# Kernel optimization log

Measured on AMD Instinct MI355X. Metric: run time of the kernel, lower is better.

The kernel has to match this reference:

```python
import jax, jax.numpy as jnp
import numpy as np

INPUT, HIDDEN, OUT = 30, 128, 11

def setup_inputs() -> dict:
    key = jax.random.key(0)
    ks = jax.random.split(key, 9)
    s_ih = 1.0 / np.sqrt(HIDDEN)
    def u(k, shape):
        return jax.random.uniform(k, shape, jnp.float32, -s_ih, s_ih)
    return {
        "x": jax.random.normal(ks[0], (4096, 256, INPUT), jnp.float32),
        "W_ih": u(ks[1], (4 * HIDDEN, INPUT)),
        "W_hh": u(ks[2], (4 * HIDDEN, HIDDEN)),
        "b_ih": u(ks[3], (4 * HIDDEN,)),
        "b_hh": u(ks[4], (4 * HIDDEN,)),
        "W0": u(ks[5], (HIDDEN, HIDDEN)),
        "b0": u(ks[6], (HIDDEN,)),
        "W1": u(ks[7], (OUT, HIDDEN)),
        "b1": u(ks[8], (OUT,)),
    }

def lstm_last_h(x, W_ih, W_hh, b_ih, b_hh):
    # x: [B, T, I]; precompute input projections for all timesteps
    B = x.shape[0]
    xg = jnp.einsum('bti,gi->btg', x, W_ih) + b_ih + b_hh  # [B, T, 4H]
    def step(carry, g_x):
        h, c = carry
        g = g_x + h @ W_hh.T  # [B, 4H]
        i, f, gg, o = jnp.split(g, 4, axis=-1)  # PyTorch gate order i,f,g,o
        i = jax.nn.sigmoid(i); f = jax.nn.sigmoid(f)
        gg = jnp.tanh(gg); o = jax.nn.sigmoid(o)
        c = f * c + i * gg
        h = o * jnp.tanh(c)
        return (h, c), None
    h0 = jnp.zeros((B, HIDDEN), x.dtype)
    c0 = jnp.zeros((B, HIDDEN), x.dtype)
    (h, c), _ = jax.lax.scan(step, (h0, c0), jnp.swapaxes(xg, 0, 1))
    return h

def reference(x, W_ih, W_hh, b_ih, b_hh, W0, b0, W1, b1):
    h = lstm_last_h(x, W_ih, W_hh, b_ih, b_hh)  # [B, H]
    y0 = jax.nn.relu(h @ W0.T + b0)
    return y0 @ W1.T + b1  # [B, 11]
```

## Files before the change

kernel.cpp:

```cpp
#include <hip/hip_runtime.h>

#define TT 256
#define II 30
#define HH 128
#define TB 16
#define HROWF 136
#define XROWF 40
#define XTT 16
#define XPANEL (XTT * TB * XROWF)

typedef _Float16 half8 __attribute__((ext_vector_type(8)));
typedef _Float16 half2v __attribute__((ext_vector_type(2)));
typedef float f32x4 __attribute__((ext_vector_type(4)));

#if __has_builtin(__builtin_amdgcn_exp2f)
#define EXP2(x) __builtin_amdgcn_exp2f(x)
#else
#define EXP2(x) exp2f(x)
#endif
#define RCP(x) __builtin_amdgcn_rcpf(x)

#define L2E 1.44269504089f
#define TWO_L2E 2.88539008177f

__device__ __forceinline__ float sig2(float a) {
  return RCP(1.0f + EXP2(-a));
}
__device__ __forceinline__ float tanh2(float a) {
  return fmaf(-2.0f, RCP(1.0f + EXP2(a)), 1.0f);
}
__device__ __forceinline__ float tanh2s(float c) {
  return tanh2(c * TWO_L2E);
}

__global__ __launch_bounds__(512, 2)
void lstm_mfma(const float* __restrict__ x,
               const float* __restrict__ W_ih,
               const float* __restrict__ W_hh,
               const float* __restrict__ b_ih,
               const float* __restrict__ b_hh,
               const float* __restrict__ W0,
               const float* __restrict__ b0v,
               const float* __restrict__ W1,
               const float* __restrict__ b1v,
               float* __restrict__ out)
{
  __shared__ __align__(16) _Float16 Hb[2][TB * HROWF];
  __shared__ __align__(16) _Float16 Xp[2][XPANEL];
  __shared__ float y0ls[TB * 132];

  const int tid = threadIdx.x;
  const int bbase = blockIdx.x * TB;
  const int wv = tid >> 6;
  const int lane = tid & 63;
  const int col = lane & 15;
  const int grp = lane >> 4;

  half8 bf[4][5];
  float bias[4];
  #pragma unroll
  for (int g = 0; g < 4; ++g) {
    const float sc = (g == 2) ? TWO_L2E : L2E;
    const int n = g * 128 + wv * 16 + col;
    #pragma unroll
    for (int ks = 0; ks < 4; ++ks) {
      const float4 p = *reinterpret_cast<const float4*>(W_hh + n * HH + ks * 32 + grp * 8);
      const float4 q = *reinterpret_cast<const float4*>(W_hh + n * HH + ks * 32 + grp * 8 + 4);
      bf[g][ks] = (half8){(_Float16)(p.x * sc), (_Float16)(p.y * sc),
                          (_Float16)(p.z * sc), (_Float16)(p.w * sc),
                          (_Float16)(q.x * sc), (_Float16)(q.y * sc),
                          (_Float16)(q.z * sc), (_Float16)(q.w * sc)};
    }
    {
      float v[8];
      #pragma unroll
      for (int j = 0; j < 8; ++j) {
        const int cc = grp * 8 + j;
        v[j] = (cc < II) ? W_ih[n * II + cc] * sc : 0.0f;
      }
      bf[g][4] = (half8){(_Float16)v[0], (_Float16)v[1], (_Float16)v[2], (_Float16)v[3],
                         (_Float16)v[4], (_Float16)v[5], (_Float16)v[6], (_Float16)v[7]};
    }
    bias[g] = (b_ih[n] + b_hh[n]) * sc;
  }

  const bool stg = (tid < 480);
  const int sS = stg ? (tid / 30) : 15;
  const int qS = tid % 30;
  const int g0 = qS * 16;
  const int tt0 = g0 / 30;
  const int i00 = g0 % 30;
  const float* wbase = x + (size_t)(bbase + sS) * (TT * II);

  float4 xr0, xr1, xr2, xr3;
  auto xload = [&](int win) {
    if (!stg) return;
    const float* p = wbase + win * (XTT * II) + g0;
    xr0 = *reinterpret_cast<const float4*>(p);
    xr1 = *reinterpret_cast<const float4*>(p + 4);
    xr2 = *reinterpret_cast<const float4*>(p + 8);
    xr3 = *reinterpret_cast<const float4*>(p + 12);
  };
  auto xwrite = [&](int dstb) {
    if (!stg) return;
    _Float16* d = &Xp[dstb][0];
    const float vv[16] = {xr0.x, xr0.y, xr0.z, xr0.w, xr1.x, xr1.y, xr1.z, xr1.w,
                          xr2.x, xr2.y, xr2.z, xr2.w, xr3.x, xr3.y, xr3.z, xr3.w};
    int tt = tt0, i = i00;
    #pragma unroll
    for (int j = 0; j < 16; ++j) {
      d[tt * (TB * XROWF) + sS * XROWF + i] = (_Float16)vv[j];
      ++i;
      if (i == II) { i = 0; ++tt; }
    }
  };

  if (tid < 256) {
    const int s = tid >> 4, u8 = (tid & 15) * 8;
    *reinterpret_cast<half8*>(&Hb[0][s * HROWF + u8]) = (half8){0,0,0,0,0,0,0,0};
  }
  {
    const int pb = tid >> 8, rr = tid & 255;
    const int tt = rr >> 4, s = rr & 15;
    *reinterpret_cast<half2v*>(&Xp[pb][tt * (TB * XROWF) + s * XROWF + II]) = (half2v){0, 0};
  }

  float c[4] = {0.0f, 0.0f, 0.0f, 0.0f};

  xload(0);
  xwrite(0);
  __syncthreads();

  auto step = [&](int tt_idx, const _Float16* Ar, _Float16* Aw, const _Float16* Xr) {
    half8 af[5];
    #pragma unroll
    for (int ks = 0; ks < 4; ++ks)
      af[ks] = *reinterpret_cast<const half8*>(&Ar[col * HROWF + ks * 32 + grp * 8]);
    af[4] = *reinterpret_cast<const half8*>(&Xr[tt_idx * (TB * XROWF) + col * XROWF + grp * 8]);

    f32x4 a0 = {bias[0], bias[0], bias[0], bias[0]};
    f32x4 a1 = {bias[1], bias[1], bias[1], bias[1]};
    #pragma unroll
    for (int ks = 0; ks < 5; ++ks)
      a0 = __builtin_amdgcn_mfma_f32_16x16x32_f16(af[ks], bf[0][ks], a0, 0, 0, 0);
    #pragma unroll
    for (int ks = 0; ks < 5; ++ks)
      a1 = __builtin_amdgcn_mfma_f32_16x16x32_f16(af[ks], bf[1][ks], a1, 0, 0, 0);

    float ig[4], fg[4];
    #pragma unroll
    for (int r = 0; r < 4; ++r) { ig[r] = sig2(a0[r]); fg[r] = sig2(a1[r]); }

    f32x4 a2 = {bias[2], bias[2], bias[2], bias[2]};
    f32x4 a3 = {bias[3], bias[3], bias[3], bias[3]};
    #pragma unroll
    for (int ks = 0; ks < 5; ++ks)
      a2 = __builtin_amdgcn_mfma_f32_16x16x32_f16(af[ks], bf[2][ks], a2, 0, 0, 0);
    #pragma unroll
    for (int ks = 0; ks < 5; ++ks)
      a3 = __builtin_amdgcn_mfma_f32_16x16x32_f16(af[ks], bf[3][ks], a3, 0, 0, 0);

    #pragma unroll
    for (int r = 0; r < 4; ++r) {
      const float tg = tanh2(a2[r]);
      const float og = sig2(a3[r]);
      const float cn = fmaf(fg[r], c[r], ig[r] * tg);
      c[r] = cn;
      Aw[(grp * 4 + r) * HROWF + wv * 16 + col] = (_Float16)(og * tanh2s(cn));
    }
    __syncthreads();
  };

  for (int win = 0; win < 16; ++win) {
    const _Float16* Xr = Xp[win & 1];
    if (win + 1 < 16) xload(win + 1);
    for (int k = 0; k < 8; k += 2) {
      step(k,     Hb[0], Hb[1], Xr);
      step(k + 1, Hb[1], Hb[0], Xr);
    }
    if (win + 1 < 16) xwrite((win + 1) & 1);
    for (int k = 8; k < 16; k += 2) {
      step(k,     Hb[0], Hb[1], Xr);
      step(k + 1, Hb[1], Hb[0], Xr);
    }
  }

  if (tid < 256) {
    const int s = tid >> 4;
    const int n0 = (tid & 15) * 8;
    float acch[8];
    #pragma unroll
    for (int nj = 0; nj < 8; ++nj) acch[nj] = b0v[n0 + nj];
    #pragma unroll
    for (int kb = 0; kb < 16; ++kb) {
      const half8 hh = *reinterpret_cast<const half8*>(&Hb[0][s * HROWF + kb * 8]);
      float hf[8];
      #pragma unroll
      for (int j = 0; j < 8; ++j) hf[j] = (float)hh[j];
      #pragma unroll
      for (int nj = 0; nj < 8; ++nj) {
        const float4 w0 = *reinterpret_cast<const float4*>(W0 + (n0 + nj) * HH + kb * 8);
        const float4 w1 = *reinterpret_cast<const float4*>(W0 + (n0 + nj) * HH + kb * 8 + 4);
        acch[nj] = fmaf(hf[0], w0.x, fmaf(hf[1], w0.y, fmaf(hf[2], w0.z, fmaf(hf[3], w0.w,
                   fmaf(hf[4], w1.x, fmaf(hf[5], w1.y, fmaf(hf[6], w1.z, fmaf(hf[7], w1.w,
                        acch[nj]))))))));
      }
    }
    #pragma unroll
    for (int nj = 0; nj < 8; ++nj)
      y0ls[s * 132 + n0 + nj] = fmaxf(acch[nj], 0.0f);
  }
  __syncthreads();

  if (tid < TB * 11) {
    const int s = tid / 11;
    const int oo = tid % 11;
    float acc1 = b1v[oo];
    const float4* y4 = reinterpret_cast<const float4*>(y0ls + s * 132);
    const float4* w4 = reinterpret_cast<const float4*>(W1 + oo * HH);
    #pragma unroll 8
    for (int k4 = 0; k4 < 32; ++k4) {
      const float4 yv = y4[k4];
      const float4 wv4 = w4[k4];
      acc1 = fmaf(yv.x, wv4.x, fmaf(yv.y, wv4.y, fmaf(yv.z, wv4.z, fmaf(yv.w, wv4.w, acc1))));
    }
    out[(size_t)(bbase + s) * 11 + oo] = acc1;
  }
}

extern "C" void kernel_launch(void* const* d_in, const int* in_sizes, int n_in,
                              void* d_out, int out_size, void* d_ws, size_t ws_size,
                              hipStream_t stream) {
  const float* x    = (const float*)d_in[0];
  const float* W_ih = (const float*)d_in[1];
  const float* W_hh = (const float*)d_in[2];
  const float* b_ih = (const float*)d_in[3];
  const float* b_hh = (const float*)d_in[4];
  const float* W0   = (const float*)d_in[5];
  const float* b0   = (const float*)d_in[6];
  const float* W1   = (const float*)d_in[7];
  const float* b1   = (const float*)d_in[8];
  float* out = (float*)d_out;
  lstm_mfma<<<256, 512, 0, stream>>>(x, W_ih, W_hh, b_ih, b_hh, W0, b0, W1, b1, out);
}
```

Baseline: 234.5 us.

## Halve batch per block to 8 rows, doubling grid and fusing gate activations

Each block now handles 8 sequences instead of 16, and the grid doubles to 512 blocks so more CUs get a serial recurrence chain, with the launch bound raised to request 4 blocks per CU. The 16-row MFMA tile is kept, so half of each tile is padding and is zeroed up front, and only lanes holding real rows run the gate math. The gate nonlinearities are merged to share reciprocals (sigmoid*tanh in one rcp) with clamped exp2 to avoid overflow. This wastes half of every MFMA, but it shortens per-block work and the cost per step is dominated by latency and syncs rather than MFMA throughput.

```diff
diff --git a/kernel.cpp b/kernel.cpp
--- a/kernel.cpp
+++ b/kernel.cpp
@@ -3,14 +3,14 @@
 #define TT 256
 #define II 30
 #define HH 128
-#define TB 16
+#define TB 8
+#define NR 16
 #define HROWF 136
 #define XROWF 40
 #define XTT 16
-#define XPANEL (XTT * TB * XROWF)
+#define XPANEL (XTT * NR * XROWF)
 
 typedef _Float16 half8 __attribute__((ext_vector_type(8)));
-typedef _Float16 half2v __attribute__((ext_vector_type(2)));
 typedef float f32x4 __attribute__((ext_vector_type(4)));
 
 #if __has_builtin(__builtin_amdgcn_exp2f)
@@ -23,17 +23,7 @@
 #define L2E 1.44269504089f
 #define TWO_L2E 2.88539008177f
 
-__device__ __forceinline__ float sig2(float a) {
-  return RCP(1.0f + EXP2(-a));
-}
-__device__ __forceinline__ float tanh2(float a) {
-  return fmaf(-2.0f, RCP(1.0f + EXP2(a)), 1.0f);
-}
-__device__ __forceinline__ float tanh2s(float c) {
-  return tanh2(c * TWO_L2E);
-}
-
-__global__ __launch_bounds__(512, 2)
+__global__ __launch_bounds__(512, 4)
 void lstm_mfma(const float* __restrict__ x,
                const float* __restrict__ W_ih,
                const float* __restrict__ W_hh,
@@ -45,7 +35,7 @@
                const float* __restrict__ b1v,
                float* __restrict__ out)
 {
-  __shared__ __align__(16) _Float16 Hb[2][TB * HROWF];
+  __shared__ __align__(16) _Float16 Hb[2][NR * HROWF];
   __shared__ __align__(16) _Float16 Xp[2][XPANEL];
   __shared__ float y0ls[TB * 132];
 
@@ -84,8 +74,8 @@
     bias[g] = (b_ih[n] + b_hh[n]) * sc;
   }
 
-  const bool stg = (tid < 480);
-  const int sS = stg ? (tid / 30) : 15;
+  const bool stg = (tid < 240);
+  const int sS = stg ? (tid / 30) : 7;
   const int qS = tid % 30;
   const int g0 = qS * 16;
   const int tt0 = g0 / 30;
@@ -109,25 +99,25 @@
     int tt = tt0, i = i00;
     #pragma unroll
     for (int j = 0; j < 16; ++j) {
-      d[tt * (TB * XROWF) + sS * XROWF + i] = (_Float16)vv[j];
+      d[tt * (NR * XROWF) + sS * XROWF + i] = (_Float16)vv[j];
       ++i;
       if (i == II) { i = 0; ++tt; }
     }
   };
 
-  if (tid < 256) {
-    const int s = tid >> 4, u8 = (tid & 15) * 8;
-    *reinterpret_cast<half8*>(&Hb[0][s * HROWF + u8]) = (half8){0,0,0,0,0,0,0,0};
-  }
   {
-    const int pb = tid >> 8, rr = tid & 255;
-    const int tt = rr >> 4, s = rr & 15;
-    *reinterpret_cast<half2v*>(&Xp[pb][tt * (TB * XROWF) + s * XROWF + II]) = (half2v){0, 0};
+    _Float16* hflat = &Hb[0][0];
+    for (int i8 = tid; i8 < (2 * NR * HROWF) / 8; i8 += 512)
+      *reinterpret_cast<half8*>(hflat + i8 * 8) = (half8){0,0,0,0,0,0,0,0};
+    _Float16* xflat = &Xp[0][0];
+    for (int i8 = tid; i8 < (2 * XPANEL) / 8; i8 += 512)
+      *reinterpret_cast<half8*>(xflat + i8 * 8) = (half8){0,0,0,0,0,0,0,0};
   }
 
   float c[4] = {0.0f, 0.0f, 0.0f, 0.0f};
 
   xload(0);
+  __syncthreads();
   xwrite(0);
   __syncthreads();
 
@@ -136,37 +126,40 @@
     #pragma unroll
     for (int ks = 0; ks < 4; ++ks)
       af[ks] = *reinterpret_cast<const half8*>(&Ar[col * HROWF + ks * 32 + grp * 8]);
-    af[4] = *reinterpret_cast<const half8*>(&Xr[tt_idx * (TB * XROWF) + col * XROWF + grp * 8]);
+    af[4] = *reinterpret_cast<const half8*>(&Xr[tt_idx * (NR * XROWF) + col * XROWF + grp * 8]);
 
     f32x4 a0 = {bias[0], bias[0], bias[0], bias[0]};
     f32x4 a1 = {bias[1], bias[1], bias[1], bias[1]};
-    #pragma unroll
-    for (int ks = 0; ks < 5; ++ks)
-      a0 = __builtin_amdgcn_mfma_f32_16x16x32_f16(af[ks], bf[0][ks], a0, 0, 0, 0);
-    #pragma unroll
-    for (int ks = 0; ks < 5; ++ks)
-      a1 = __builtin_amdgcn_mfma_f32_16x16x32_f16(af[ks], bf[1][ks], a1, 0, 0, 0);
-
-    float ig[4], fg[4];
-    #pragma unroll
-    for (int r = 0; r < 4; ++r) { ig[r] = sig2(a0[r]); fg[r] = sig2(a1[r]); }
-
     f32x4 a2 = {bias[2], bias[2], bias[2], bias[2]};
     f32x4 a3 = {bias[3], bias[3], bias[3], bias[3]};
     #pragma unroll
     for (int ks = 0; ks < 5; ++ks)
+      a0 = __builtin_amdgcn_mfma_f32_16x16x32_f16(af[ks], bf[0][ks], a0, 0, 0, 0);
+    #pragma unroll
+    for (int ks = 0; ks < 5; ++ks)
+      a1 = __builtin_amdgcn_mfma_f32_16x16x32_f16(af[ks], bf[1][ks], a1, 0, 0, 0);
+    #pragma unroll
+    for (int ks = 0; ks < 5; ++ks)
       a2 = __builtin_amdgcn_mfma_f32_16x16x32_f16(af[ks], bf[2][ks], a2, 0, 0, 0);
     #pragma unroll
     for (int ks = 0; ks < 5; ++ks)
       a3 = __builtin_amdgcn_mfma_f32_16x16x32_f16(af[ks], bf[3][ks], a3, 0, 0, 0);
 
-    #pragma unroll
-    for (int r = 0; r < 4; ++r) {
-      const float tg = tanh2(a2[r]);
-      const float og = sig2(a3[r]);
-      const float cn = fmaf(fg[r], c[r], ig[r] * tg);
-      c[r] = cn;
-      Aw[(grp * 4 + r) * HROWF + wv * 16 + col] = (_Float16)(og * tanh2s(cn));
+    if (grp < 2) {
+      #pragma unroll
+      for (int r = 0; r < 4; ++r) {
+        const float Ei = EXP2(-a0[r]);
+        const float Ef = EXP2(-a1[r]);
+        const float Eg = EXP2(fminf(a2[r], 126.0f));
+        const float Eo = EXP2(-a3[r]);
+        const float ig = (Eg - 1.0f) * RCP((1.0f + Ei) * (Eg + 1.0f));
+        const float ff = RCP(1.0f + Ef);
+        const float cn = fmaf(ff, c[r], ig);
+        c[r] = cn;
+        const float Ec = EXP2(fminf(cn * TWO_L2E, 126.0f));
+        const float oth = (Ec - 1.0f) * RCP((1.0f + Eo) * (Ec + 1.0f));
+        Aw[(grp * 4 + r) * HROWF + wv * 16 + col] = (_Float16)oth;
+      }
     }
     __syncthreads();
   };
@@ -185,7 +178,7 @@
     }
   }
 
-  if (tid < 256) {
+  if (tid < TB * 16) {
     const int s = tid >> 4;
     const int n0 = (tid & 15) * 8;
     float acch[8];
@@ -241,5 +234,5 @@
   const float* W1   = (const float*)d_in[7];
   const float* b1   = (const float*)d_in[8];
   float* out = (float*)d_out;
-  lstm_mfma<<<256, 512, 0, stream>>>(x, W_ih, W_hh, b_ih, b_hh, W0, b0, W1, b1, out);
+  lstm_mfma<<<512, 512, 0, stream>>>(x, W_ih, W_hh, b_ih, b_hh, W0, b0, W1, b1, out);
 }
```

Measured after the change: 571.0 us. +143.4%, slower.
